# Kernel tuning notes

Measured on AMD Instinct MI355X. Metric: run time of the kernel, lower is better.

Reference implementation:

```python
import jax, jax.numpy as jnp
import numpy as np

N = 20000   # num_perts (nodes)
E = 640000  # edges
H = 2       # attention heads
D = 64      # hidden_dim = out_dim
L = 4       # num_layers
NEG_SLOPE_ATT = 0.2    # GATv2 attention leaky_relu
NEG_SLOPE_ACT = 0.01   # F.leaky_relu default


def setup_inputs() -> dict:
    key = jax.random.key(0)
    ks = jax.random.split(key, 9)
    s = 0.1
    return {
        "edge_index": jax.random.randint(ks[0], (2, E), 0, N, dtype=jnp.int64 if jax.config.x64_enabled else jnp.int32),
        "edge_weight": jax.random.uniform(ks[1], (E,), jnp.float32),
        "pert_emb": jax.random.normal(ks[2], (N, D), jnp.float32) * s,
        "Wl": jax.random.normal(ks[3], (L, D, H * D), jnp.float32) * s,
        "bl": jnp.zeros((L, H * D), jnp.float32),
        "Wr": jax.random.normal(ks[4], (L, D, H * D), jnp.float32) * s,
        "br": jnp.zeros((L, H * D), jnp.float32),
        "att": jax.random.normal(ks[5], (L, H, D), jnp.float32) * s,
        "bias": jnp.zeros((L, D), jnp.float32),
        "Wo": jax.random.normal(ks[6], (D, D), jnp.float32) * s,
        "bo": jnp.zeros((D,), jnp.float32),
    }


def _gatv2_layer(x, src, dst, Wl, bl, Wr, br, att, bias):
    # x: [N, D] -> out: [N, D] (heads averaged, concat=False)
    xl = (x @ Wl + bl).reshape(N, H, D)  # source transform
    xr = (x @ Wr + br).reshape(N, H, D)  # target transform
    e = jax.nn.leaky_relu(xl[src] + xr[dst], NEG_SLOPE_ATT)        # [E,H,D]
    logits = jnp.einsum('ehd,hd->eh', e, att)                      # [E,H]
    # segment softmax over incoming edges per target node
    m = jax.ops.segment_max(logits, dst, num_segments=N)           # [N,H]
    m = jnp.where(jnp.isfinite(m), m, 0.0)
    ex = jnp.exp(logits - m[dst])
    denom = jax.ops.segment_sum(ex, dst, num_segments=N)           # [N,H]
    alpha = ex / (denom[dst] + 1e-16)                              # [E,H]
    msg = xl[src] * alpha[:, :, None]                              # [E,H,D]
    out = jax.ops.segment_sum(msg, dst, num_segments=N)            # [N,H,D]
    return out.mean(axis=1) + bias                                 # [N,D]


def reference(edge_index, edge_weight, pert_emb, Wl, bl, Wr, br, att, bias, Wo, bo):
    del edge_weight  # use_edge_weight=False -> edge_weight set to None
    src, dst = edge_index[0], edge_index[1]
    x = pert_emb  # embedding lookup of arange(num_perts) == full table
    for i in range(L):
        x = _gatv2_layer(x, src, dst, Wl[i], bl[i], Wr[i], br[i], att[i], bias[i])
        x = jax.nn.leaky_relu(x, NEG_SLOPE_ACT)  # dropout p=0.0 is identity
    x = x @ Wo + bo
    x = jax.nn.leaky_relu(x, NEG_SLOPE_ACT)
    return x
```

## Files before the change

### kernel.cpp

```cpp
#include <hip/hip_runtime.h>
#include <hip/hip_fp16.h>
#include <math.h>
#include <float.h>

#define NN 20000
#define EE 640000
#define HH 2
#define DD 64
#define LL 4
#define HD 128
#define CAP 80
#define GR 32
#define GEMM_BLOCKS (NN / GR)
#define SCAT_BLOCKS ((EE + 255) / 256)
#define NPB 4
#define LOG2E 1.4426950408889634f

typedef _Float16 half4 __attribute__((ext_vector_type(4)));

__device__ __forceinline__ float4 h2f(half4 h) {
    return make_float4((float)h.x, (float)h.y, (float)h.z, (float)h.w);
}
__device__ __forceinline__ half4 f2h(float a, float b, float c, float d) {
    half4 r;
    r.x = (_Float16)a; r.y = (_Float16)b; r.z = (_Float16)c; r.w = (_Float16)d;
    return r;
}


__device__ __forceinline__ float row16_sum(float x) {
    int t;
    t = __builtin_amdgcn_update_dpp(0, __float_as_int(x), 0xB1, 0xF, 0xF, true);
    x += __int_as_float(t);
    t = __builtin_amdgcn_update_dpp(0, __float_as_int(x), 0x4E, 0xF, 0xF, true);
    x += __int_as_float(t);
    t = __builtin_amdgcn_update_dpp(0, __float_as_int(x), 0x124, 0xF, 0xF, true);
    x += __int_as_float(t);
    t = __builtin_amdgcn_update_dpp(0, __float_as_int(x), 0x128, 0xF, 0xF, true);
    x += __int_as_float(t);
    return x;
}

__device__ __forceinline__ float att_dot(float4 xv, float4 xrv, float4 atv) {
    float4 v;
    v.x = xv.x + xrv.x; v.y = xv.y + xrv.y; v.z = xv.z + xrv.z; v.w = xv.w + xrv.w;
    v.x = fmaxf(v.x, 0.f) + 0.2f * fminf(v.x, 0.f);
    v.y = fmaxf(v.y, 0.f) + 0.2f * fminf(v.y, 0.f);
    v.z = fmaxf(v.z, 0.f) + 0.2f * fminf(v.z, 0.f);
    v.w = fmaxf(v.w, 0.f) + 0.2f * fminf(v.w, 0.f);
    return fmaf(v.x, atv.x, fmaf(v.y, atv.y, fmaf(v.z, atv.z, v.w * atv.w)));
}

__global__ void __launch_bounds__(256) prep_kernel(
        const float* __restrict__ x,
        const float* __restrict__ Wl, const float* __restrict__ bl,
        const float* __restrict__ Wr, const float* __restrict__ br,
        _Float16* __restrict__ xl, _Float16* __restrict__ xr,
        const int* __restrict__ src, const int* __restrict__ dst,
        int* __restrict__ cnt, int* __restrict__ csr_src) {
    int tid = threadIdx.x;
    if (blockIdx.x >= GEMM_BLOCKS) {
        int e = (blockIdx.x - GEMM_BLOCKS) * 256 + tid;
        if (e < EE) {
            int d = dst[e];
            int pos = atomicAdd(&cnt[d], 1);
            if (pos < CAP) csr_src[d * CAP + pos] = src[e];
        }
        return;
    }
    __shared__ float xs[16][GR];
    __shared__ float ws[16][2 * HD];
    int row0 = blockIdx.x * GR;
    int tc = tid & 63;
    int tr = tid >> 6;
    int c0 = tc * 4;

    float4 bv;
    {
        const float* bsrc = (c0 < HD) ? (bl + c0) : (br + (c0 - HD));
        bv = *(const float4*)bsrc;
    }
    float acc[8][4];
#pragma unroll
    for (int r = 0; r < 8; ++r) {
        acc[r][0] = bv.x; acc[r][1] = bv.y; acc[r][2] = bv.z; acc[r][3] = bv.w;
    }

    int sr = tid >> 3;
    int skk = (tid & 7) * 2;

    for (int kc = 0; kc < DD; kc += 16) {
        __syncthreads();
        {
            float2 v = *(const float2*)&x[(size_t)(row0 + sr) * DD + kc + skk];
            xs[skk][sr] = v.x;
            xs[skk + 1][sr] = v.y;
        }
#pragma unroll
        for (int q = 0; q < 4; ++q) {
            int idx = tid + 256 * q;
            int kk = idx >> 6;
            int cc = (idx & 63) * 4;
            const float* srcp = (cc < HD) ? (Wl + (size_t)(kc + kk) * HD + cc)
                                          : (Wr + (size_t)(kc + kk) * HD + (cc - HD));
            *(float4*)&ws[kk][cc] = *(const float4*)srcp;
        }
        __syncthreads();
#pragma unroll
        for (int kk = 0; kk < 16; ++kk) {
            float4 wv = *(const float4*)&ws[kk][c0];
            float xv[8];
            *(float4*)&xv[0] = *(const float4*)&xs[kk][tr * 8];
            *(float4*)&xv[4] = *(const float4*)&xs[kk][tr * 8 + 4];
#pragma unroll
            for (int r = 0; r < 8; ++r) {
                acc[r][0] = fmaf(xv[r], wv.x, acc[r][0]);
                acc[r][1] = fmaf(xv[r], wv.y, acc[r][1]);
                acc[r][2] = fmaf(xv[r], wv.z, acc[r][2]);
                acc[r][3] = fmaf(xv[r], wv.w, acc[r][3]);
            }
        }
    }

    _Float16* ybase = (c0 < HD) ? xl : xr;
    int cw = (c0 < HD) ? c0 : (c0 - HD);
#pragma unroll
    for (int r = 0; r < 8; ++r) {
        int row = row0 + tr * 8 + r;
        *(half4*)&ybase[(size_t)row * HD + cw] =
            f2h(acc[r][0], acc[r][1], acc[r][2], acc[r][3]);
    }
}

template <bool FINAL>
__global__ void __launch_bounds__(256, 4) fused_aggregate(
        const _Float16* __restrict__ xl, const _Float16* __restrict__ xr,
        const float* __restrict__ att, const int* __restrict__ cnt,
        const int* __restrict__ csr_src, const float* __restrict__ bias,
        const float* __restrict__ Wnl, const float* __restrict__ bnl,
        const float* __restrict__ Wnr, const float* __restrict__ bnr,
        const float* __restrict__ Wo, const float* __restrict__ bo,
        _Float16* __restrict__ xlo, _Float16* __restrict__ xro,
        float* __restrict__ out) {
    int tid = threadIdx.x;
    int lane = tid & 63;
    int w = tid >> 6;
    int node = blockIdx.x * NPB + w;
    int g = lane >> 4;
    int fo = (lane & 15) * 4;

    __shared__ float sh_o[NPB][DD];
    __shared__ float wst[16][2 * HD];
    __shared__ int   sh_idx[NPB][CAP];

    int start = node * CAP;
    int deg = min(cnt[node], CAP);

    if (lane < CAP / 2) {
        *(int2*)&sh_idx[w][lane * 2] = *(const int2*)&csr_src[start + lane * 2];
    }

    unsigned nrow = (unsigned)node << 7;
    const float4 xra = h2f(*(const half4*)&xr[nrow + fo]);
    const float4 xrb = h2f(*(const half4*)&xr[nrow + 64 + fo]);
    float4 ata = *(const float4*)&att[fo];
    float4 atb = *(const float4*)&att[64 + fo];
    ata.x *= LOG2E; ata.y *= LOG2E; ata.z *= LOG2E; ata.w *= LOG2E;
    atb.x *= LOG2E; atb.y *= LOG2E; atb.z *= LOG2E; atb.w *= LOG2E;

    float sa = 0.f, sb = 0.f;
    float4 aa = {0.f, 0.f, 0.f, 0.f};
    float4 ab = {0.f, 0.f, 0.f, 0.f};

    if (deg > 0) {
        int niter = (deg + 7) >> 3;

#define IDX2(k) (*(const int2*)&sh_idx[w][8 * min((k), CAP / 8 - 1) + 2 * g])

#define GATHER(B0a, B0b, B1a, B1b, k)                                      \
        {                                                                  \
            int2 r_ = IDX2(k);                                             \
            int sl_ = 8 * (k) + 2 * g;                                     \
            int s0_ = (sl_ < deg) ? r_.x : 0;                              \
            int s1_ = (sl_ + 1 < deg) ? r_.y : 0;                          \
            unsigned q0_ = (unsigned)s0_ << 7, q1_ = (unsigned)s1_ << 7;   \
            B0a = *(const half4*)&xl[q0_ + fo];                            \
            B0b = *(const half4*)&xl[q0_ + 64 + fo];                       \
            B1a = *(const half4*)&xl[q1_ + fo];                            \
            B1b = *(const half4*)&xl[q1_ + 64 + fo];                       \
        }

#define COMPUTE(B0a, B0b, B1a, B1b, k)                                     \
        {                                                                  \
            float4 x0a = h2f(B0a), x0b = h2f(B0b);                         \
            float4 x1a = h2f(B1a), x1b = h2f(B1b);                         \
            float t0a = row16_sum(att_dot(x0a, xra, ata));                 \
            float t0b = row16_sum(att_dot(x0b, xrb, atb));                 \
            float t1a = row16_sum(att_dot(x1a, xra, ata));                 \
            float t1b = row16_sum(att_dot(x1b, xrb, atb));                 \
            int sl_ = 8 * (k) + 2 * g;                                     \
            float w0a = (sl_ < deg) ? exp2f(t0a) : 0.f;                    \
            float w1a = (sl_ + 1 < deg) ? exp2f(t1a) : 0.f;                \
            float w0b = (sl_ < deg) ? exp2f(t0b) : 0.f;                    \
            float w1b = (sl_ + 1 < deg) ? exp2f(t1b) : 0.f;                \
            sa += w0a + w1a;                                               \
            sb += w0b + w1b;                                               \
            aa.x = fmaf(w0a, x0a.x, fmaf(w1a, x1a.x, aa.x));               \
            aa.y = fmaf(w0a, x0a.y, fmaf(w1a, x1a.y, aa.y));               \
            aa.z = fmaf(w0a, x0a.z, fmaf(w1a, x1a.z, aa.z));               \
            aa.w = fmaf(w0a, x0a.w, fmaf(w1a, x1a.w, aa.w));               \
            ab.x = fmaf(w0b, x0b.x, fmaf(w1b, x1b.x, ab.x));               \
            ab.y = fmaf(w0b, x0b.y, fmaf(w1b, x1b.y, ab.y));               \
            ab.z = fmaf(w0b, x0b.z, fmaf(w1b, x1b.z, ab.z));               \
            ab.w = fmaf(w0b, x0b.w, fmaf(w1b, x1b.w, ab.w));               \
        }

        half4 A0a, A0b, A1a, A1b;
        half4 B0a, B0b, B1a, B1b;
        half4 C0a, C0b, C1a, C1b;
        half4 D0a, D0b, D1a, D1b;

        GATHER(A0a, A0b, A1a, A1b, 0);
        GATHER(B0a, B0b, B1a, B1b, 1);
        GATHER(C0a, C0b, C1a, C1b, 2);

        int it = 0;
        while (true) {
            {
                GATHER(D0a, D0b, D1a, D1b, it + 3);
                __builtin_amdgcn_sched_barrier(0);
                COMPUTE(A0a, A0b, A1a, A1b, it);
            }
            if (++it == niter) break;
            {
                GATHER(A0a, A0b, A1a, A1b, it + 3);
                __builtin_amdgcn_sched_barrier(0);
                COMPUTE(B0a, B0b, B1a, B1b, it);
            }
            if (++it == niter) break;
            {
                GATHER(B0a, B0b, B1a, B1b, it + 3);
                __builtin_amdgcn_sched_barrier(0);
                COMPUTE(C0a, C0b, C1a, C1b, it);
            }
            if (++it == niter) break;
            {
                GATHER(C0a, C0b, C1a, C1b, it + 3);
                __builtin_amdgcn_sched_barrier(0);
                COMPUTE(D0a, D0b, D1a, D1b, it);
            }
            if (++it == niter) break;
        }
#undef IDX2
#undef GATHER
#undef COMPUTE
    }

#pragma unroll
    for (int off = 16; off <= 32; off <<= 1) {
        sa += __shfl_xor(sa, off);
        aa.x += __shfl_xor(aa.x, off);
        aa.y += __shfl_xor(aa.y, off);
        aa.z += __shfl_xor(aa.z, off);
        aa.w += __shfl_xor(aa.w, off);
        sb += __shfl_xor(sb, off);
        ab.x += __shfl_xor(ab.x, off);
        ab.y += __shfl_xor(ab.y, off);
        ab.z += __shfl_xor(ab.z, off);
        ab.w += __shfl_xor(ab.w, off);
    }

    float inva = 1.0f / (sa + 1e-16f);
    float invb = 1.0f / (sb + 1e-16f);

    if (lane < 16) {
        const float4 bv = *(const float4*)&bias[fo];
        float4 o;
        o.x = fmaf(0.5f, fmaf(aa.x, inva, ab.x * invb), bv.x);
        o.y = fmaf(0.5f, fmaf(aa.y, inva, ab.y * invb), bv.y);
        o.z = fmaf(0.5f, fmaf(aa.z, inva, ab.z * invb), bv.z);
        o.w = fmaf(0.5f, fmaf(aa.w, inva, ab.w * invb), bv.w);
        o.x = o.x > 0.f ? o.x : 0.01f * o.x;
        o.y = o.y > 0.f ? o.y : 0.01f * o.y;
        o.z = o.z > 0.f ? o.z : 0.01f * o.z;
        o.w = o.w > 0.f ? o.w : 0.01f * o.w;
        *(float4*)&sh_o[w][fo] = o;
    }

    if (FINAL) {
        float* wlin = &wst[0][0];
        {
            int idx = tid * 16;
            *(float4*)&wlin[idx]      = *(const float4*)&Wo[idx];
            *(float4*)&wlin[idx + 4]  = *(const float4*)&Wo[idx + 4];
            *(float4*)&wlin[idx + 8]  = *(const float4*)&Wo[idx + 8];
            *(float4*)&wlin[idx + 12] = *(const float4*)&Wo[idx + 12];
        }
        __syncthreads();
        int j = lane;
        float acc = bo[j];
#pragma unroll 8
        for (int k = 0; k < DD; ++k) {
            acc = fmaf(sh_o[w][k], wlin[k * DD + j], acc);
        }
        acc = acc > 0.f ? acc : 0.01f * acc;
        out[(size_t)node * DD + j] = acc;
    } else {
        int c0 = lane * 4;
        float4 acc4;
        {
            const float* bsrc = (c0 < HD) ? (bnl + c0) : (bnr + (c0 - HD));
            acc4 = *(const float4*)bsrc;
        }
        for (int kc = 0; kc < DD; kc += 16) {
            __syncthreads();
#pragma unroll
            for (int q = 0; q < 4; ++q) {
                int idx = tid + 256 * q;
                int kk = idx >> 6;
                int cc = (idx & 63) * 4;
                const float* p = (cc < HD) ? (Wnl + (size_t)(kc + kk) * HD + cc)
                                           : (Wnr + (size_t)(kc + kk) * HD + (cc - HD));
                *(float4*)&wst[kk][cc] = *(const float4*)p;
            }
            __syncthreads();
#pragma unroll
            for (int kk = 0; kk < 16; ++kk) {
                float xo = sh_o[w][kc + kk];
                float4 wv = *(const float4*)&wst[kk][c0];
                acc4.x = fmaf(xo, wv.x, acc4.x);
                acc4.y = fmaf(xo, wv.y, acc4.y);
                acc4.z = fmaf(xo, wv.z, acc4.z);
                acc4.w = fmaf(xo, wv.w, acc4.w);
            }
        }
        half4 hv = f2h(acc4.x, acc4.y, acc4.z, acc4.w);
        if (c0 < HD) *(half4*)&xlo[(size_t)node * HD + c0] = hv;
        else         *(half4*)&xro[(size_t)node * HD + (c0 - HD)] = hv;
    }
}

extern "C" void kernel_launch(void* const* d_in, const int* in_sizes, int n_in,
                              void* d_out, int out_size, void* d_ws, size_t ws_size,
                              hipStream_t stream) {
    const int* edge_index = (const int*)d_in[0];
    const int* src = edge_index;
    const int* dst = edge_index + EE;
    const float* pert = (const float*)d_in[2];
    const float* Wl = (const float*)d_in[3];
    const float* bl = (const float*)d_in[4];
    const float* Wr = (const float*)d_in[5];
    const float* br = (const float*)d_in[6];
    const float* att = (const float*)d_in[7];
    const float* bias = (const float*)d_in[8];
    const float* Wo = (const float*)d_in[9];
    const float* bo = (const float*)d_in[10];
    float* out = (float*)d_out;

    char* w = (char*)d_ws;
    _Float16* xlA = (_Float16*)w;     w += (size_t)NN * HD * 2;
    _Float16* xrA = (_Float16*)w;     w += (size_t)NN * HD * 2;
    _Float16* xlB = (_Float16*)w;     w += (size_t)NN * HD * 2;
    _Float16* xrB = (_Float16*)w;     w += (size_t)NN * HD * 2;
    int* cnt = (int*)w;               w += (size_t)NN * 4;
    int* csr_src = (int*)w;           w += (size_t)NN * CAP * 4;

    hipMemsetAsync(cnt, 0, (size_t)NN * 4, stream);
    prep_kernel<<<GEMM_BLOCKS + SCAT_BLOCKS, 256, 0, stream>>>(
        pert, Wl, bl, Wr, br, xlA, xrA, src, dst, cnt, csr_src);

    _Float16* xls[2] = {xlA, xlB};
    _Float16* xrs[2] = {xrA, xrB};
    for (int l = 0; l < LL - 1; ++l) {
        fused_aggregate<false><<<NN / NPB, 256, 0, stream>>>(
            xls[l & 1], xrs[l & 1], att + (size_t)l * HD, cnt, csr_src,
            bias + (size_t)l * DD,
            Wl + (size_t)(l + 1) * DD * HD, bl + (size_t)(l + 1) * HD,
            Wr + (size_t)(l + 1) * DD * HD, br + (size_t)(l + 1) * HD,
            nullptr, nullptr,
            xls[(l + 1) & 1], xrs[(l + 1) & 1], nullptr);
    }
    fused_aggregate<true><<<NN / NPB, 256, 0, stream>>>(
        xls[(LL - 1) & 1], xrs[(LL - 1) & 1], att + (size_t)(LL - 1) * HD, cnt, csr_src,
        bias + (size_t)(LL - 1) * DD,
        nullptr, nullptr, nullptr, nullptr,
        Wo, bo, nullptr, nullptr, out);
}
```

Measured before the change: 285.4 us.

## Use half8 gathers with head-per-half-row lane mapping and prefetch next-layer weights

Each 16-lane row now holds both heads of an edge: lanes 0-7 take head 0 and lanes 8-15 take head 1, each loading 8 halves as one 16-byte gather instead of two 8-byte loads. The attention dot-product reduction shrinks to a 3-step DPP reduction over 8 lanes, and the two heads are combined with an xor-8 shuffle before the output. The next-layer and output weight tiles are also loaded into registers before the cross-row reduction and double-buffered across k-chunks, so global-load latency overlaps other work. This raises register use (8-wide accumulators plus prefetch buffers), which may lower occupancy.

```diff
diff --git a/kernel.cpp b/kernel.cpp
--- a/kernel.cpp
+++ b/kernel.cpp
@@ -17,38 +17,23 @@
 #define LOG2E 1.4426950408889634f
 
 typedef _Float16 half4 __attribute__((ext_vector_type(4)));
-
-__device__ __forceinline__ float4 h2f(half4 h) {
-    return make_float4((float)h.x, (float)h.y, (float)h.z, (float)h.w);
-}
+typedef _Float16 half8 __attribute__((ext_vector_type(8)));
+
 __device__ __forceinline__ half4 f2h(float a, float b, float c, float d) {
     half4 r;
     r.x = (_Float16)a; r.y = (_Float16)b; r.z = (_Float16)c; r.w = (_Float16)d;
     return r;
 }
 
-
-__device__ __forceinline__ float row16_sum(float x) {
+__device__ __forceinline__ float grp8_sum(float x) {
     int t;
     t = __builtin_amdgcn_update_dpp(0, __float_as_int(x), 0xB1, 0xF, 0xF, true);
     x += __int_as_float(t);
     t = __builtin_amdgcn_update_dpp(0, __float_as_int(x), 0x4E, 0xF, 0xF, true);
     x += __int_as_float(t);
-    t = __builtin_amdgcn_update_dpp(0, __float_as_int(x), 0x124, 0xF, 0xF, true);
-    x += __int_as_float(t);
-    t = __builtin_amdgcn_update_dpp(0, __float_as_int(x), 0x128, 0xF, 0xF, true);
+    t = __builtin_amdgcn_update_dpp(0, __float_as_int(x), 0x141, 0xF, 0xF, true);
     x += __int_as_float(t);
     return x;
-}
-
-__device__ __forceinline__ float att_dot(float4 xv, float4 xrv, float4 atv) {
-    float4 v;
-    v.x = xv.x + xrv.x; v.y = xv.y + xrv.y; v.z = xv.z + xrv.z; v.w = xv.w + xrv.w;
-    v.x = fmaxf(v.x, 0.f) + 0.2f * fminf(v.x, 0.f);
-    v.y = fmaxf(v.y, 0.f) + 0.2f * fminf(v.y, 0.f);
-    v.z = fmaxf(v.z, 0.f) + 0.2f * fminf(v.z, 0.f);
-    v.w = fmaxf(v.w, 0.f) + 0.2f * fminf(v.w, 0.f);
-    return fmaf(v.x, atv.x, fmaf(v.y, atv.y, fmaf(v.z, atv.z, v.w * atv.w)));
 }
 
 __global__ void __launch_bounds__(256) prep_kernel(
@@ -147,7 +132,8 @@
     int w = tid >> 6;
     int node = blockIdx.x * NPB + w;
     int g = lane >> 4;
-    int fo = (lane & 15) * 4;
+    int hl = lane & 15;
+    int eo = hl * 8;
 
     __shared__ float sh_o[NPB][DD];
     __shared__ float wst[16][2 * HD];
@@ -161,93 +147,96 @@
     }
 
     unsigned nrow = (unsigned)node << 7;
-    const float4 xra = h2f(*(const half4*)&xr[nrow + fo]);
-    const float4 xrb = h2f(*(const half4*)&xr[nrow + 64 + fo]);
-    float4 ata = *(const float4*)&att[fo];
-    float4 atb = *(const float4*)&att[64 + fo];
-    ata.x *= LOG2E; ata.y *= LOG2E; ata.z *= LOG2E; ata.w *= LOG2E;
-    atb.x *= LOG2E; atb.y *= LOG2E; atb.z *= LOG2E; atb.w *= LOG2E;
-
-    float sa = 0.f, sb = 0.f;
-    float4 aa = {0.f, 0.f, 0.f, 0.f};
-    float4 ab = {0.f, 0.f, 0.f, 0.f};
+
+    float xr8[8], at8[8];
+    {
+        half8 xh = *(const half8*)&xr[nrow + eo];
+        float4 a0 = *(const float4*)&att[eo];
+        float4 a1 = *(const float4*)&att[eo + 4];
+#pragma unroll
+        for (int t = 0; t < 8; ++t) xr8[t] = (float)xh[t];
+        at8[0] = a0.x * LOG2E; at8[1] = a0.y * LOG2E;
+        at8[2] = a0.z * LOG2E; at8[3] = a0.w * LOG2E;
+        at8[4] = a1.x * LOG2E; at8[5] = a1.y * LOG2E;
+        at8[6] = a1.z * LOG2E; at8[7] = a1.w * LOG2E;
+    }
+
+    float s = 0.f;
+    float acc[8] = {0.f, 0.f, 0.f, 0.f, 0.f, 0.f, 0.f, 0.f};
 
     if (deg > 0) {
         int niter = (deg + 7) >> 3;
 
 #define IDX2(k) (*(const int2*)&sh_idx[w][8 * min((k), CAP / 8 - 1) + 2 * g])
 
-#define GATHER(B0a, B0b, B1a, B1b, k)                                      \
+#define GATHER(H0, H1, k)                                                  \
         {                                                                  \
             int2 r_ = IDX2(k);                                             \
             int sl_ = 8 * (k) + 2 * g;                                     \
             int s0_ = (sl_ < deg) ? r_.x : 0;                              \
             int s1_ = (sl_ + 1 < deg) ? r_.y : 0;                          \
-            unsigned q0_ = (unsigned)s0_ << 7, q1_ = (unsigned)s1_ << 7;   \
-            B0a = *(const half4*)&xl[q0_ + fo];                            \
-            B0b = *(const half4*)&xl[q0_ + 64 + fo];                       \
-            B1a = *(const half4*)&xl[q1_ + fo];                            \
-            B1b = *(const half4*)&xl[q1_ + 64 + fo];                       \
-        }
-
-#define COMPUTE(B0a, B0b, B1a, B1b, k)                                     \
+            H0 = *(const half8*)&xl[((unsigned)s0_ << 7) + eo];            \
+            H1 = *(const half8*)&xl[((unsigned)s1_ << 7) + eo];            \
+        }
+
+#define COMPUTE(H0, H1, k)                                                 \
         {                                                                  \
-            float4 x0a = h2f(B0a), x0b = h2f(B0b);                         \
-            float4 x1a = h2f(B1a), x1b = h2f(B1b);                         \
-            float t0a = row16_sum(att_dot(x0a, xra, ata));                 \
-            float t0b = row16_sum(att_dot(x0b, xrb, atb));                 \
-            float t1a = row16_sum(att_dot(x1a, xra, ata));                 \
-            float t1b = row16_sum(att_dot(x1b, xrb, atb));                 \
+            float x0[8], x1[8];                                            \
+            _Pragma("unroll")                                              \
+            for (int t = 0; t < 8; ++t) {                                  \
+                x0[t] = (float)H0[t]; x1[t] = (float)H1[t];                \
+            }                                                              \
+            float t0 = 0.f, t1 = 0.f;                                      \
+            _Pragma("unroll")                                              \
+            for (int t = 0; t < 8; ++t) {                                  \
+                float v0 = x0[t] + xr8[t];                                 \
+                v0 = fmaxf(v0, 0.f) + 0.2f * fminf(v0, 0.f);               \
+                t0 = fmaf(v0, at8[t], t0);                                 \
+                float v1 = x1[t] + xr8[t];                                 \
+                v1 = fmaxf(v1, 0.f) + 0.2f * fminf(v1, 0.f);               \
+                t1 = fmaf(v1, at8[t], t1);                                 \
+            }                                                              \
+            t0 = grp8_sum(t0);                                             \
+            t1 = grp8_sum(t1);                                             \
             int sl_ = 8 * (k) + 2 * g;                                     \
-            float w0a = (sl_ < deg) ? exp2f(t0a) : 0.f;                    \
-            float w1a = (sl_ + 1 < deg) ? exp2f(t1a) : 0.f;                \
-            float w0b = (sl_ < deg) ? exp2f(t0b) : 0.f;                    \
-            float w1b = (sl_ + 1 < deg) ? exp2f(t1b) : 0.f;                \
-            sa += w0a + w1a;                                               \
-            sb += w0b + w1b;                                               \
-            aa.x = fmaf(w0a, x0a.x, fmaf(w1a, x1a.x, aa.x));               \
-            aa.y = fmaf(w0a, x0a.y, fmaf(w1a, x1a.y, aa.y));               \
-            aa.z = fmaf(w0a, x0a.z, fmaf(w1a, x1a.z, aa.z));               \
-            aa.w = fmaf(w0a, x0a.w, fmaf(w1a, x1a.w, aa.w));               \
-            ab.x = fmaf(w0b, x0b.x, fmaf(w1b, x1b.x, ab.x));               \
-            ab.y = fmaf(w0b, x0b.y, fmaf(w1b, x1b.y, ab.y));               \
-            ab.z = fmaf(w0b, x0b.z, fmaf(w1b, x1b.z, ab.z));               \
-            ab.w = fmaf(w0b, x0b.w, fmaf(w1b, x1b.w, ab.w));               \
-        }
-
-        half4 A0a, A0b, A1a, A1b;
-        half4 B0a, B0b, B1a, B1b;
-        half4 C0a, C0b, C1a, C1b;
-        half4 D0a, D0b, D1a, D1b;
-
-        GATHER(A0a, A0b, A1a, A1b, 0);
-        GATHER(B0a, B0b, B1a, B1b, 1);
-        GATHER(C0a, C0b, C1a, C1b, 2);
+            float w0 = (sl_ < deg) ? exp2f(t0) : 0.f;                      \
+            float w1 = (sl_ + 1 < deg) ? exp2f(t1) : 0.f;                  \
+            s += w0 + w1;                                                  \
+            _Pragma("unroll")                                              \
+            for (int t = 0; t < 8; ++t)                                    \
+                acc[t] = fmaf(w0, x0[t], fmaf(w1, x1[t], acc[t]));         \
+        }
+
+        half8 A0, A1, B0, B1, C0, C1, D0, D1;
+
+        GATHER(A0, A1, 0);
+        GATHER(B0, B1, 1);
+        GATHER(C0, C1, 2);
 
         int it = 0;
         while (true) {
             {
-                GATHER(D0a, D0b, D1a, D1b, it + 3);
+                GATHER(D0, D1, it + 3);
                 __builtin_amdgcn_sched_barrier(0);
-                COMPUTE(A0a, A0b, A1a, A1b, it);
+                COMPUTE(A0, A1, it);
             }
             if (++it == niter) break;
             {
-                GATHER(A0a, A0b, A1a, A1b, it + 3);
+                GATHER(A0, A1, it + 3);
                 __builtin_amdgcn_sched_barrier(0);
-                COMPUTE(B0a, B0b, B1a, B1b, it);
+                COMPUTE(B0, B1, it);
             }
             if (++it == niter) break;
             {
-                GATHER(B0a, B0b, B1a, B1b, it + 3);
+                GATHER(B0, B1, it + 3);
                 __builtin_amdgcn_sched_barrier(0);
-                COMPUTE(C0a, C0b, C1a, C1b, it);
+                COMPUTE(C0, C1, it);
             }
             if (++it == niter) break;
             {
-                GATHER(C0a, C0b, C1a, C1b, it + 3);
+                GATHER(C0, C1, it + 3);
                 __builtin_amdgcn_sched_barrier(0);
-                COMPUTE(D0a, D0b, D1a, D1b, it);
+                COMPUTE(D0, D1, it);
             }
             if (++it == niter) break;
         }
@@ -256,55 +245,71 @@
 #undef COMPUTE
     }
 
+    float4 pf[4];
+    if (FINAL) {
+        int idx = tid * 16;
+        pf[0] = *(const float4*)&Wo[idx];
+        pf[1] = *(const float4*)&Wo[idx + 4];
+        pf[2] = *(const float4*)&Wo[idx + 8];
+        pf[3] = *(const float4*)&Wo[idx + 12];
+    } else {
+#pragma unroll
+        for (int q = 0; q < 4; ++q) {
+            int idx = tid + 256 * q;
+            int kk = idx >> 6;
+            int cc = (idx & 63) * 4;
+            const float* p = (cc < HD) ? (Wnl + (size_t)kk * HD + cc)
+                                       : (Wnr + (size_t)kk * HD + (cc - HD));
+            pf[q] = *(const float4*)p;
+        }
+    }
+
 #pragma unroll
     for (int off = 16; off <= 32; off <<= 1) {
-        sa += __shfl_xor(sa, off);
-        aa.x += __shfl_xor(aa.x, off);
-        aa.y += __shfl_xor(aa.y, off);
-        aa.z += __shfl_xor(aa.z, off);
-        aa.w += __shfl_xor(aa.w, off);
-        sb += __shfl_xor(sb, off);
-        ab.x += __shfl_xor(ab.x, off);
-        ab.y += __shfl_xor(ab.y, off);
-        ab.z += __shfl_xor(ab.z, off);
-        ab.w += __shfl_xor(ab.w, off);
-    }
-
-    float inva = 1.0f / (sa + 1e-16f);
-    float invb = 1.0f / (sb + 1e-16f);
-
-    if (lane < 16) {
-        const float4 bv = *(const float4*)&bias[fo];
-        float4 o;
-        o.x = fmaf(0.5f, fmaf(aa.x, inva, ab.x * invb), bv.x);
-        o.y = fmaf(0.5f, fmaf(aa.y, inva, ab.y * invb), bv.y);
-        o.z = fmaf(0.5f, fmaf(aa.z, inva, ab.z * invb), bv.z);
-        o.w = fmaf(0.5f, fmaf(aa.w, inva, ab.w * invb), bv.w);
-        o.x = o.x > 0.f ? o.x : 0.01f * o.x;
-        o.y = o.y > 0.f ? o.y : 0.01f * o.y;
-        o.z = o.z > 0.f ? o.z : 0.01f * o.z;
-        o.w = o.w > 0.f ? o.w : 0.01f * o.w;
-        *(float4*)&sh_o[w][fo] = o;
+        s += __shfl_xor(s, off);
+#pragma unroll
+        for (int t = 0; t < 8; ++t) acc[t] += __shfl_xor(acc[t], off);
+    }
+
+    float so = __shfl_xor(s, 8);
+    float oth[8];
+#pragma unroll
+    for (int t = 0; t < 8; ++t) oth[t] = __shfl_xor(acc[t], 8);
+
+    if (lane < 8) {
+        float inv0 = 1.0f / (s + 1e-16f);
+        float inv1 = 1.0f / (so + 1e-16f);
+        float4 bv0 = *(const float4*)&bias[lane * 8];
+        float4 bv1 = *(const float4*)&bias[lane * 8 + 4];
+        float bv[8] = {bv0.x, bv0.y, bv0.z, bv0.w, bv1.x, bv1.y, bv1.z, bv1.w};
+        float o[8];
+#pragma unroll
+        for (int t = 0; t < 8; ++t) {
+            float v = fmaf(0.5f, fmaf(acc[t], inv0, oth[t] * inv1), bv[t]);
+            o[t] = v > 0.f ? v : 0.01f * v;
+        }
+        *(float4*)&sh_o[w][lane * 8]     = make_float4(o[0], o[1], o[2], o[3]);
+        *(float4*)&sh_o[w][lane * 8 + 4] = make_float4(o[4], o[5], o[6], o[7]);
     }
 
     if (FINAL) {
         float* wlin = &wst[0][0];
         {
             int idx = tid * 16;
-            *(float4*)&wlin[idx]      = *(const float4*)&Wo[idx];
-            *(float4*)&wlin[idx + 4]  = *(const float4*)&Wo[idx + 4];
-            *(float4*)&wlin[idx + 8]  = *(const float4*)&Wo[idx + 8];
-            *(float4*)&wlin[idx + 12] = *(const float4*)&Wo[idx + 12];
+            *(float4*)&wlin[idx]      = pf[0];
+            *(float4*)&wlin[idx + 4]  = pf[1];
+            *(float4*)&wlin[idx + 8]  = pf[2];
+            *(float4*)&wlin[idx + 12] = pf[3];
         }
         __syncthreads();
         int j = lane;
-        float acc = bo[j];
+        float og = bo[j];
 #pragma unroll 8
         for (int k = 0; k < DD; ++k) {
-            acc = fmaf(sh_o[w][k], wlin[k * DD + j], acc);
-        }
-        acc = acc > 0.f ? acc : 0.01f * acc;
-        out[(size_t)node * DD + j] = acc;
+            og = fmaf(sh_o[w][k], wlin[k * DD + j], og);
+        }
+        og = og > 0.f ? og : 0.01f * og;
+        out[(size_t)node * DD + j] = og;
     } else {
         int c0 = lane * 4;
         float4 acc4;
@@ -319,9 +324,19 @@
                 int idx = tid + 256 * q;
                 int kk = idx >> 6;
                 int cc = (idx & 63) * 4;
-                const float* p = (cc < HD) ? (Wnl + (size_t)(kc + kk) * HD + cc)
-                                           : (Wnr + (size_t)(kc + kk) * HD + (cc - HD));
-                *(float4*)&wst[kk][cc] = *(const float4*)p;
+                *(float4*)&wst[kk][cc] = pf[q];
+            }
+            if (kc + 16 < DD) {
+#pragma unroll
+                for (int q = 0; q < 4; ++q) {
+                    int idx = tid + 256 * q;
+                    int kk = idx >> 6;
+                    int cc = (idx & 63) * 4;
+                    const float* p = (cc < HD)
+                        ? (Wnl + (size_t)(kc + 16 + kk) * HD + cc)
+                        : (Wnr + (size_t)(kc + 16 + kk) * HD + (cc - HD));
+                    pf[q] = *(const float4*)p;
+                }
             }
             __syncthreads();
 #pragma unroll
```

Result: slower. 459.0 us (+60.8%).
